# Kernel tuning notes

Measured on AMD Instinct MI355X. Metric: run time of the kernel, lower is better.

The kernel has to match this reference:

```python
import math
import jax, jax.numpy as jnp
import numpy as np

B, S, D = 2, 1024, 4096
H, DH = 32, 128


def setup_inputs() -> dict:
    key = jax.random.key(0)
    ks = jax.random.split(key, 8)
    scale = 1.0 / math.sqrt(D)
    return {
        "hidden_q": jax.random.normal(ks[0], (B, S, D), jnp.float32),
        "hidden_kv": jax.random.normal(ks[1], (B, S, D), jnp.float32),
        "attention_mask": jax.random.randint(ks[2], (B, S, S), 0, 2) > 0,
        "position_bias": jax.random.normal(ks[3], (B, H, S, S), jnp.float32),
        "Wq": jax.random.normal(ks[4], (D, H * DH), jnp.float32) * scale,
        "Wk": jax.random.normal(ks[5], (D, H * DH), jnp.float32) * scale,
        "Wv": jax.random.normal(ks[6], (D, H * DH), jnp.float32) * scale,
        "Wo": jax.random.normal(ks[7], (H * DH, D), jnp.float32) * scale,
    }


def reference(hidden_q, hidden_kv, attention_mask, position_bias, Wq, Wk, Wv, Wo):
    b, len_q, _ = hidden_q.shape
    len_k = hidden_kv.shape[1]
    # projections -> [B, H, S, DH]
    q = (hidden_q @ Wq).reshape(b, len_q, H, DH).transpose(0, 2, 1, 3)
    k = (hidden_kv @ Wk).reshape(b, len_k, H, DH).transpose(0, 2, 1, 3)
    v = (hidden_kv @ Wv).reshape(b, len_k, H, DH).transpose(0, 2, 1, 3)
    # scores [B, H, Q, K]
    score = jnp.einsum("bhqd,bhkd->bhqk", q, k) / math.sqrt(DH)
    score = score + position_bias
    mask = attention_mask[:, None, :, :]  # [B,1,Q,K]
    score = jnp.where(mask, score, -jnp.inf)
    probs = jax.nn.softmax(score, axis=-1)
    probs = jnp.where(mask, probs, 0.0)  # post-softmax mask (also kills NaN rows)
    ctx = jnp.einsum("bhqk,bhkd->bhqd", probs, v)
    ctx = ctx.transpose(0, 2, 1, 3).reshape(b, len_q, H * DH)
    out = ctx @ Wo
    return out
```

## Files before the change

### kernel.cpp

```cpp
#include <hip/hip_runtime.h>
#include <stdint.h>


#define B_  2
#define S_  1024
#define D_  4096
#define H_  32
#define DH_ 128
#define M_  (B_ * S_)
#define KSTR 8192

typedef __attribute__((ext_vector_type(8))) short bf16x8;
typedef __attribute__((ext_vector_type(8))) unsigned short u16x8;
typedef __attribute__((ext_vector_type(4))) float f32x4;

static __device__ __forceinline__ unsigned short f32_to_bf16(float f) {
    unsigned int x = __float_as_uint(f);
    x += 0x7fffu + ((x >> 16) & 1u);
    return (unsigned short)(x >> 16);
}

static __device__ __forceinline__ f32x4 mfma16(bf16x8 a, bf16x8 b, f32x4 c) {
    return __builtin_amdgcn_mfma_f32_16x16x32_bf16(a, b, c, 0, 0, 0);
}

#if defined(__has_builtin)
#if __has_builtin(__builtin_amdgcn_global_load_lds)
#define HAVE_GLOAD_LDS 1
#endif
#endif

#ifdef HAVE_GLOAD_LDS
#define GLD16(g, lbase, lane)                                                  \
    __builtin_amdgcn_global_load_lds(                                          \
        (const __attribute__((address_space(1))) void*)(g),                    \
        (__attribute__((address_space(3))) void*)(lbase), 16, 0, 0)
#else
#define GLD16(g, lbase, lane)                                                  \
    do { *(bf16x8*)((unsigned short*)(lbase) + (size_t)(lane) * 8) =           \
             *(const bf16x8*)(g); } while (0)
#endif

__global__ void detect_mask_kernel(const unsigned char* __restrict__ m, int* flag) {
    int l = threadIdx.x;
    uint4 v = ((const uint4*)m)[l];
    unsigned int ww[4] = {v.x, v.y, v.z, v.w};
    int nz_hi = 0, nz_lo01 = 0;
#pragma unroll
    for (int wi = 0; wi < 4; ++wi)
#pragma unroll
        for (int bi = 0; bi < 4; ++bi) {
            unsigned int byte = (ww[wi] >> (bi * 8)) & 0xffu;
            if (byte && bi != 0) nz_hi = 1;
            if (byte && bi <= 1) nz_lo01 = 1;
        }
    int any_hi = __any(nz_hi);
    int any_lo01 = __any(nz_lo01);
    if (l == 0) *flag = (!any_hi) ? 1 : ((!any_lo01) ? 2 : 0);
}

__global__ void canon_mask_kernel(const void* __restrict__ m, const int* __restrict__ flag,
                                  unsigned char* __restrict__ out, int n) {
    int i = blockIdx.x * 256 + threadIdx.x;
    if (i >= n) return;
    int f = *flag;
    unsigned char v;
    if (f == 1)      v = (unsigned char)(((const int*)m)[i] != 0);
    else if (f == 2) v = (unsigned char)(((const float*)m)[i] != 0.0f);
    else             v = (unsigned char)(((const unsigned char*)m)[i] != 0);
    out[i] = v;
}

__global__ void cvt2_bf16_kernel(const float* __restrict__ a, const float* __restrict__ b,
                                 unsigned short* __restrict__ oa, unsigned short* __restrict__ ob) {
    int i = blockIdx.x * 256 + threadIdx.x;
    const int n4 = (B_ * S_ * D_) / 4;
    const float* src = (i < n4) ? a : b;
    unsigned short* dst = (i < n4) ? oa : ob;
    int j = (i < n4) ? i : i - n4;
    float4 v = ((const float4*)src)[j];
    ushort4 o;
    o.x = f32_to_bf16(v.x); o.y = f32_to_bf16(v.y);
    o.z = f32_to_bf16(v.z); o.w = f32_to_bf16(v.w);
    ((ushort4*)dst)[j] = o;
}

__global__ __launch_bounds__(256) void transpose_all_kernel(
        const float* __restrict__ Wq, const float* __restrict__ Wk,
        const float* __restrict__ Wv, const float* __restrict__ Wo,
        unsigned short* __restrict__ WTq, unsigned short* __restrict__ WTkv,
        unsigned short* __restrict__ WTo) {
    __shared__ unsigned short lds[64][65];
    int which = blockIdx.x >> 12;
    int bid = blockIdx.x & 4095;
    const float* W = (which == 0) ? Wq : (which == 1) ? Wk : (which == 2) ? Wv : Wo;
    unsigned short* WT = (which == 0) ? WTq
                       : (which == 1) ? WTkv
                       : (which == 2) ? (WTkv + (size_t)4096 * 4096)
                                      : WTo;
    int bx = bid & 63;
    int by = bid >> 6;
    int t = threadIdx.x;
    int tr = t >> 4;
    int tc = (t & 15) * 4;
#pragma unroll
    for (int p = 0; p < 4; ++p) {
        int r = p * 16 + tr;
        float4 v = *(const float4*)(W + (size_t)(by * 64 + r) * D_ + bx * 64 + tc);
        lds[r][tc + 0] = f32_to_bf16(v.x);
        lds[r][tc + 1] = f32_to_bf16(v.y);
        lds[r][tc + 2] = f32_to_bf16(v.z);
        lds[r][tc + 3] = f32_to_bf16(v.w);
    }
    __syncthreads();
    int wn = t >> 3;
    int k0 = (t & 7) * 8;
#pragma unroll
    for (int p2 = 0; p2 < 2; ++p2) {
        int n = p2 * 32 + wn;
        u16x8 o;
#pragma unroll
        for (int j = 0; j < 8; ++j) o[j] = lds[k0 + j][n];
        *(u16x8*)(WT + (size_t)(bx * 64 + n) * D_ + by * 64 + k0) = o;
    }
}

__global__ __launch_bounds__(256) void vt_kernel(const unsigned short* __restrict__ KV,
                                                 unsigned short* __restrict__ Vtw) {
    __shared__ unsigned short lds[64][72];
    int bid = blockIdx.x;
    int dt = bid & 1;
    int st = (bid >> 1) & 15;
    int h  = (bid >> 5) & 31;
    int b  = bid >> 10;
    int t = threadIdx.x;
    int r = t >> 2;
    int c0 = (t & 3) * 16;
    const unsigned short* src =
        KV + (size_t)(b * S_ + st * 64 + r) * KSTR + 4096 + h * DH_ + dt * 64 + c0;
    bf16x8 v0 = *(const bf16x8*)(src);
    bf16x8 v1 = *(const bf16x8*)(src + 8);
    *(bf16x8*)&lds[r][c0] = v0;
    *(bf16x8*)&lds[r][c0 + 8] = v1;
    __syncthreads();
    unsigned short tmp[16];
#pragma unroll
    for (int i = 0; i < 16; ++i) tmp[i] = lds[c0 + i][r];
    unsigned short* dst =
        Vtw + ((size_t)((b * H_ + h) * DH_ + dt * 64 + r)) * S_ + st * 64 + c0;
    *(bf16x8*)dst = *(bf16x8*)&tmp[0];
    *(bf16x8*)(dst + 8) = *(bf16x8*)&tmp[8];
}

__device__ __forceinline__ void gemm_core(const unsigned short* __restrict__ A,
                                          const unsigned short* __restrict__ BT,
                                          void* __restrict__ C, int out_f32,
                                          int m0, int n0, int cstride,
                                          int koff, int NT, char* ldsc) {
    const int t = threadIdx.x;
    const int w = t >> 6, l = t & 63;
    const int lr = l & 15, lg = l >> 4;
    const int wmh = w >> 2;
    const int walf = w & 3;
    const int wm = wmh << 7;
    const int wn = walf << 6;

    const int ca0 = lg ^ (lr & 7);
    const int aoff0 = lr * 128 + (ca0 << 4);
    const int aoff1 = lr * 128 + ((ca0 ^ 4) << 4);
    const int boff0 = ((walf & 1) * 64 + lr) * 128 + (ca0 << 4);
    const int boff1 = ((walf & 1) * 64 + lr) * 128 + ((ca0 ^ 4) << 4);

    const int srow = t >> 3;
    const int sch = (t & 7) ^ (srow & 7);
    const size_t soff0 = (size_t)srow * 4096 + (size_t)(sch << 3);
    const size_t soff1 = soff0 + (size_t)64 * 4096;
    const int ldso = w << 10;

    f32x4 ac[8][4];
    f32x4 vzero = {0.f, 0.f, 0.f, 0.f};
#pragma unroll
    for (int i = 0; i < 8; ++i)
#pragma unroll
        for (int j = 0; j < 4; ++j) ac[i][j] = vzero;

#define STAGE_ELEM(E, SS)                                                      \
    do {                                                                       \
        int er_ = (E) & 3;                                                     \
        const unsigned short* mb_ = (er_ < 2)                                  \
            ? A + (size_t)(m0 + ((er_ & 1) << 7)) * 4096                       \
            : BT + (size_t)(n0 + ((er_ & 1) << 7)) * 4096;                     \
        mb_ += (size_t)((((E) >> 2) << 6) + koff);                             \
        char* d0_ = ldsc + (SS) * 16384 + ldso;                                \
        GLD16(mb_ + soff0, d0_, l);                                            \
        GLD16(mb_ + soff1, d0_ + 8192, l);                                     \
    } while (0)

#pragma unroll
    for (int e = 0; e < 6; ++e) STAGE_ELEM(e, e);

    const int NT4 = NT << 2;
    int E = 6, ss = 6, s0 = 0;
    bf16x8 bfr[4][2];

#pragma unroll 1
    for (int tau = 0; tau < NT; ++tau) {
        int sA = s0 + wmh;             if (sA >= 10) sA -= 10;
        int sB = s0 + 2 + (walf >> 1); if (sB >= 10) sB -= 10;
        const char* pA0 = ldsc + sA * 16384 + aoff0;
        const char* pA1 = ldsc + sA * 16384 + aoff1;
        const char* pB0 = ldsc + sB * 16384 + boff0;
        const char* pB1 = ldsc + sB * 16384 + boff1;
#pragma unroll
        for (int r = 0; r < 4; ++r) {
            if (r == 0) {
                if (tau == NT - 1)
                    asm volatile("s_waitcnt vmcnt(0)" ::: "memory");
                else
                    asm volatile("s_waitcnt vmcnt(4)" ::: "memory");
            }
            __builtin_amdgcn_s_barrier();
            asm volatile("" ::: "memory");
            if (r == 0) {
#pragma unroll
                for (int nf = 0; nf < 4; ++nf) {
                    bfr[nf][0] = *(const bf16x8*)(pB0 + nf * 2048);
                    bfr[nf][1] = *(const bf16x8*)(pB1 + nf * 2048);
                }
            }
            bf16x8 af[2][2];
            int mfb = r << 1;
#pragma unroll
            for (int j = 0; j < 2; ++j) {
                af[j][0] = *(const bf16x8*)(pA0 + (mfb + j) * 2048);
                af[j][1] = *(const bf16x8*)(pA1 + (mfb + j) * 2048);
            }
            if (E < NT4) STAGE_ELEM(E, ss);
            ++E; ss = (ss == 9) ? 0 : ss + 1;
            __builtin_amdgcn_s_setprio(1);
#pragma unroll
            for (int j = 0; j < 2; ++j)
#pragma unroll
                for (int nf = 0; nf < 4; ++nf) {
                    ac[mfb + j][nf] = mfma16(af[j][0], bfr[nf][0], ac[mfb + j][nf]);
                    ac[mfb + j][nf] = mfma16(af[j][1], bfr[nf][1], ac[mfb + j][nf]);
                }
            __builtin_amdgcn_s_setprio(0);
        }
        s0 += 4; if (s0 >= 10) s0 -= 10;
    }
#undef STAGE_ELEM

#pragma unroll
    for (int mf = 0; mf < 8; ++mf)
#pragma unroll
        for (int nf = 0; nf < 4; ++nf)
#pragma unroll
            for (int q = 0; q < 4; ++q) {
                int row = m0 + wm + mf * 16 + lg * 4 + q;
                int col = n0 + wn + nf * 16 + lr;
                if (out_f32)
                    ((float*)C)[(size_t)row * cstride + col] = ac[mf][nf][q];
                else
                    ((unsigned short*)C)[(size_t)row * cstride + col] = f32_to_bf16(ac[mf][nf][q]);
            }
}

__global__ __launch_bounds__(512, 1) void gemm_qkv_kernel(
        const unsigned short* __restrict__ Aq, const unsigned short* __restrict__ Bq,
        float* __restrict__ Pq,
        const unsigned short* __restrict__ Akv, const unsigned short* __restrict__ Bkv,
        unsigned short* __restrict__ Ckv) {
    __shared__ char ldsbuf[10 * 16384];
    int bid = blockIdx.x;
    if (bid < 256) {
        int bm = bid & 7, bn = bid >> 3;
        gemm_core(Akv, Bkv, Ckv, 0, bm << 8, bn << 8, 8192, 0, 64, ldsbuf);
    } else {
        int e = bid - 256;
        int bm = e & 7;
        int rest = e >> 3;
        int bn = rest & 15;
        int ks = rest >> 4;
        gemm_core(Aq, Bq, Pq + (size_t)ks * M_ * D_, 1, bm << 8, bn << 8, 4096,
                  ks * 2048, 32, ldsbuf);
    }
}

__global__ void reduce_q_kernel(const float* __restrict__ P, unsigned short* __restrict__ out) {
    int i = blockIdx.x * 256 + threadIdx.x;
    float4 a = ((const float4*)P)[i];
    float4 b = ((const float4*)(P + (size_t)M_ * D_))[i];
    ushort4 o;
    o.x = f32_to_bf16(a.x + b.x); o.y = f32_to_bf16(a.y + b.y);
    o.z = f32_to_bf16(a.z + b.z); o.w = f32_to_bf16(a.w + b.w);
    ((ushort4*)out)[i] = o;
}

__global__ __launch_bounds__(512, 1) void gemm_o_kernel(
        const unsigned short* __restrict__ A, const unsigned short* __restrict__ BT,
        float* __restrict__ P) {
    __shared__ char ldsbuf[10 * 16384];
    int bid = blockIdx.x;
    int bm = bid & 7;
    int rest = bid >> 3;
    int bn = rest & 15;
    int ks = rest >> 4;
    gemm_core(A, BT, P + (size_t)ks * M_ * D_, 1, bm << 8, bn << 8, 4096,
              ks * 2048, 32, ldsbuf);
}

__global__ void reduce_o_kernel(const float* __restrict__ P, float* __restrict__ out) {
    int i = blockIdx.x * 256 + threadIdx.x;
    float4 a = ((const float4*)P)[i];
    float4 b = ((const float4*)(P + (size_t)M_ * D_))[i];
    float4 o; o.x = a.x + b.x; o.y = a.y + b.y; o.z = a.z + b.z; o.w = a.w + b.w;
    ((float4*)out)[i] = o;
}

#define NEGF (-1e30f)
__global__ __launch_bounds__(256, 2) void attn_kernel(const unsigned short* __restrict__ Qw,
                                                      const unsigned short* __restrict__ KV,
                                                      const unsigned short* __restrict__ Vtw,
                                                      const float* __restrict__ bias,
                                                      const unsigned char* __restrict__ maskc,
                                                      unsigned short* __restrict__ ctx) {
    __shared__ unsigned short Kbuf[2][64 * 128];
    __shared__ unsigned short Vbuf[2][128 * 64];
    __shared__ unsigned short Plds[4][16 * 72];

    int x = blockIdx.x;
    int xcd = x & 7;
    int rest = x >> 3;
    int qt = rest & 15;
    int gq = rest >> 4;
    int g = gq * 8 + xcd;
    int b = g >> 5, h = g & 31;

    int t = threadIdx.x, w = t >> 6, l = t & 63;
    int lr = l & 15, lg = l >> 4;
    int q0 = (qt << 6) + (w << 4);

    bf16x8 qf[4];
    const unsigned short* Qp = Qw + ((size_t)(b * S_ + q0 + lr)) * D_ + h * DH_ + lg * 8;
#pragma unroll
    for (int kf = 0; kf < 4; ++kf) qf[kf] = *(const bf16x8*)(Qp + kf * 32);

    f32x4 o[8];
    f32x4 vzero = {0.f, 0.f, 0.f, 0.f};
#pragma unroll
    for (int i = 0; i < 8; ++i) o[i] = vzero;
    float m_run = NEGF, l_run = 0.f;

    const float* biasp = bias + (((size_t)(b * H_ + h)) << 20)
                              + (((size_t)(q0 + lr)) << 10);
    const unsigned char* mp = maskc + ((size_t)b << 20)
                              + (((size_t)(q0 + lr)) << 10);
    const unsigned short* Kg = KV + (size_t)(b * S_) * KSTR + h * DH_;
    const unsigned short* Vg = Vtw + (((size_t)(b * H_ + h)) * DH_) * S_;

    float4 br0[4], br1[4];
    unsigned int mr0[4], mr1[4];

#define STAGE_KV(KT, BUF)                                                          \
    do { int kv0_ = (KT) << 6;                                                     \
        _Pragma("unroll")                                                          \
        for (int c = 0; c < 4; ++c) {                                              \
            int seg = (w << 2) + c;                                                \
            int krow = (seg << 2) + (l >> 4);                                      \
            int kch = (l & 15) ^ (krow & 7);                                       \
            GLD16(Kg + (size_t)(kv0_ + krow) * KSTR + (kch << 3),                  \
                  &Kbuf[BUF][seg << 9], l);                                        \
            int vrow = (seg << 3) + (l >> 3);                                      \
            int vch = (l & 7) ^ (vrow & 7);                                        \
            GLD16(Vg + (size_t)vrow * S_ + kv0_ + (vch << 3),                      \
                  &Vbuf[BUF][seg << 9], l);                                        \
        }                                                                          \
    } while (0)

#define LOAD_BM(BR, MR, KT)                                                        \
    do { int kv0_ = (KT) << 6;                                                     \
        _Pragma("unroll")                                                          \
        for (int nb = 0; nb < 4; ++nb) {                                           \
            BR[nb] = *(const float4*)(biasp + kv0_ + (nb << 4) + (lg << 2));       \
            MR[nb] = *(const unsigned int*)(mp + kv0_ + (nb << 4) + (lg << 2));    \
        }                                                                          \
    } while (0)

#define COMPUTE(BUF, BR, MR)                                                       \
    do {                                                                           \
        f32x4 s_[4];                                                               \
        __builtin_amdgcn_s_setprio(1);                                             \
        _Pragma("unroll")                                                          \
        for (int nb = 0; nb < 4; ++nb) {                                           \
            s_[nb] = vzero;                                                        \
            int krow = (nb << 4) + lr;                                             \
            _Pragma("unroll")                                                      \
            for (int kf = 0; kf < 4; ++kf) {                                       \
                int ba = ((krow << 8) + (((kf << 5) + (lg << 3)) << 1))            \
                         ^ ((krow & 7) << 4);                                      \
                bf16x8 kfr = *(const bf16x8*)((const char*)Kbuf[BUF] + ba);        \
                s_[nb] = mfma16(kfr, qf[kf], s_[nb]);                              \
            }                                                                      \
        }                                                                          \
        __builtin_amdgcn_s_setprio(0);                                             \
        float sv[4][4];                                                            \
        _Pragma("unroll")                                                          \
        for (int nb = 0; nb < 4; ++nb) {                                           \
            float bb[4] = {BR[nb].x, BR[nb].y, BR[nb].z, BR[nb].w};                \
            _Pragma("unroll")                                                      \
            for (int r = 0; r < 4; ++r) {                                          \
                float x2 = fmaf(s_[nb][r], 0.08838834764831845f, bb[r]);           \
                sv[nb][r] = ((MR[nb] >> (r * 8)) & 0xffu) ? x2 : NEGF;             \
            }                                                                      \
        }                                                                          \
        float mt = sv[0][0];                                                       \
        _Pragma("unroll")                                                          \
        for (int nb = 0; nb < 4; ++nb)                                             \
            _Pragma("unroll")                                                      \
            for (int r = 0; r < 4; ++r) mt = fmaxf(mt, sv[nb][r]);                 \
        mt = fmaxf(mt, __shfl_xor(mt, 16, 64));                                    \
        mt = fmaxf(mt, __shfl_xor(mt, 32, 64));                                    \
        float mn = fmaxf(m_run, mt);                                               \
        float al = __expf(m_run - mn);                                             \
        m_run = mn;                                                                \
        float rs = 0.f;                                                            \
        _Pragma("unroll")                                                          \
        for (int nb = 0; nb < 4; ++nb)                                             \
            _Pragma("unroll")                                                      \
            for (int r = 0; r < 4; ++r) {                                          \
                sv[nb][r] = __expf(sv[nb][r] - m_run);                             \
                rs += sv[nb][r];                                                   \
            }                                                                      \
        rs += __shfl_xor(rs, 16, 64);                                              \
        rs += __shfl_xor(rs, 32, 64);                                              \
        l_run = l_run * al + rs;                                                   \
        float alm[4];                                                              \
        _Pragma("unroll")                                                          \
        for (int r = 0; r < 4; ++r) alm[r] = __shfl(al, (lg << 2) + r, 64);        \
        _Pragma("unroll")                                                          \
        for (int nb2 = 0; nb2 < 8; ++nb2) {                                        \
            o[nb2][0] *= alm[0]; o[nb2][1] *= alm[1];                              \
            o[nb2][2] *= alm[2]; o[nb2][3] *= alm[3];                              \
        }                                                                          \
        _Pragma("unroll")                                                          \
        for (int nb = 0; nb < 4; ++nb)                                             \
            _Pragma("unroll")                                                      \
            for (int r = 0; r < 4; ++r)                                            \
                Plds[w][lr * 72 + (nb << 4) + (lg << 2) + r] = f32_to_bf16(sv[nb][r]); \
        __builtin_amdgcn_s_setprio(1);                                             \
        _Pragma("unroll")                                                          \
        for (int kf2 = 0; kf2 < 2; ++kf2) {                                        \
            bf16x8 pf = *(const bf16x8*)&Plds[w][lr * 72 + (kf2 << 5) + (lg << 3)]; \
            _Pragma("unroll")                                                      \
            for (int nb2 = 0; nb2 < 8; ++nb2) {                                    \
                int dh = (nb2 << 4) + lr;                                          \
                int ba = ((dh << 7) + (((kf2 << 5) + (lg << 3)) << 1))             \
                         ^ ((dh & 7) << 4);                                        \
                bf16x8 vf = *(const bf16x8*)((const char*)Vbuf[BUF] + ba);         \
                o[nb2] = mfma16(pf, vf, o[nb2]);                                   \
            }                                                                      \
        }                                                                          \
        __builtin_amdgcn_s_setprio(0);                                             \
    } while (0)

    STAGE_KV(0, 0);
    LOAD_BM(br0, mr0, 0);

#pragma unroll 1
    for (int kt = 0; kt < 16; kt += 2) {
        __syncthreads();
        STAGE_KV(kt + 1, 1);
        LOAD_BM(br1, mr1, kt + 1);
        COMPUTE(0, br0, mr0);
        __syncthreads();
        if (kt < 14) {
            STAGE_KV(kt + 2, 0);
            LOAD_BM(br0, mr0, kt + 2);
        }
        COMPUTE(1, br1, mr1);
    }

    float lm[4];
#pragma unroll
    for (int r = 0; r < 4; ++r) lm[r] = __shfl(l_run, (lg << 2) + r, 64);
#pragma unroll
    for (int r = 0; r < 4; ++r) {
        float inv = lm[r] > 0.f ? 1.0f / lm[r] : 0.f;
        int q = q0 + (lg << 2) + r;
        unsigned short* cp = ctx + ((size_t)(b * S_ + q)) * D_ + h * DH_ + lr;
#pragma unroll
        for (int nb2 = 0; nb2 < 8; ++nb2)
            cp[nb2 * 16] = f32_to_bf16(o[nb2][r] * inv);
    }
#undef STAGE_KV
#undef LOAD_BM
#undef COMPUTE
}

extern "C" void kernel_launch(void* const* d_in, const int* in_sizes, int n_in,
                              void* d_out, int out_size, void* d_ws, size_t ws_size,
                              hipStream_t stream) {
    const float* hq   = (const float*)d_in[0];
    const float* hkv  = (const float*)d_in[1];
    const void*  mask = d_in[2];
    const float* bias = (const float*)d_in[3];
    const float* Wq   = (const float*)d_in[4];
    const float* Wk   = (const float*)d_in[5];
    const float* Wv   = (const float*)d_in[6];
    const float* Wo   = (const float*)d_in[7];
    float* out = (float*)d_out;

    char* ws = (char*)d_ws;
    unsigned char* mask_c = (unsigned char*)ws;
    int* flag             = (int*)(ws + (2u << 20));
    unsigned short* hq_b  = (unsigned short*)(ws + (2u << 20) + 4096);
    unsigned short* hkv_b = hq_b + ((size_t)1 << 23);
    unsigned short* WTq   = hkv_b + ((size_t)1 << 23);
    unsigned short* WTo   = WTq + ((size_t)1 << 24);
    unsigned short* WTkv  = WTo + ((size_t)1 << 24);
    unsigned short* Qws   = WTkv + ((size_t)1 << 25);
    unsigned short* KVws  = Qws + ((size_t)1 << 23);
    unsigned short* Cws   = KVws + ((size_t)1 << 24);
    unsigned short* Vtw   = Cws + ((size_t)1 << 23);
    float* Pws            = (float*)(Vtw + ((size_t)1 << 23));

    detect_mask_kernel<<<1, 64, 0, stream>>>((const unsigned char*)mask, flag);
    canon_mask_kernel<<<8192, 256, 0, stream>>>(mask, flag, mask_c, B_ * S_ * S_);
    cvt2_bf16_kernel<<<16384, 256, 0, stream>>>(hq, hkv, hq_b, hkv_b);
    transpose_all_kernel<<<16384, 256, 0, stream>>>(Wq, Wk, Wv, Wo, WTq, WTkv, WTo);

    gemm_qkv_kernel<<<512, 512, 0, stream>>>(hq_b, WTq, Pws, hkv_b, WTkv, KVws);
    reduce_q_kernel<<<(M_ * D_) / 1024, 256, 0, stream>>>(Pws, Qws);

    vt_kernel<<<B_ * H_ * 16 * 2, 256, 0, stream>>>(KVws, Vtw);
    attn_kernel<<<B_ * H_ * (S_ / 64), 256, 0, stream>>>(Qws, KVws, Vtw, bias, mask_c, Cws);

    gemm_o_kernel<<<256, 512, 0, stream>>>(Cws, WTo, Pws);
    reduce_o_kernel<<<(M_ * D_) / 1024, 256, 0, stream>>>(Pws, out);
}
```

Baseline: 500.0 us.

## Process two query tiles per attention block and merge small prep kernels

New measurement: 590.8 us. 1.18x slower.

```diff
diff --git a/kernel.cpp b/kernel.cpp
--- a/kernel.cpp
+++ b/kernel.cpp
@@ -41,29 +41,30 @@
              *(const bf16x8*)(g); } while (0)
 #endif
 
-__global__ void detect_mask_kernel(const unsigned char* __restrict__ m, int* flag) {
-    int l = threadIdx.x;
-    uint4 v = ((const uint4*)m)[l];
-    unsigned int ww[4] = {v.x, v.y, v.z, v.w};
-    int nz_hi = 0, nz_lo01 = 0;
-#pragma unroll
-    for (int wi = 0; wi < 4; ++wi)
-#pragma unroll
-        for (int bi = 0; bi < 4; ++bi) {
-            unsigned int byte = (ww[wi] >> (bi * 8)) & 0xffu;
-            if (byte && bi != 0) nz_hi = 1;
-            if (byte && bi <= 1) nz_lo01 = 1;
-        }
-    int any_hi = __any(nz_hi);
-    int any_lo01 = __any(nz_lo01);
-    if (l == 0) *flag = (!any_hi) ? 1 : ((!any_lo01) ? 2 : 0);
-}
-
-__global__ void canon_mask_kernel(const void* __restrict__ m, const int* __restrict__ flag,
+__global__ void canon_mask_kernel(const void* __restrict__ m,
                                   unsigned char* __restrict__ out, int n) {
-    int i = blockIdx.x * 256 + threadIdx.x;
+    __shared__ int sflag;
+    int t = threadIdx.x;
+    if (t < 64) {
+        uint4 v = ((const uint4*)m)[t];
+        unsigned int ww[4] = {v.x, v.y, v.z, v.w};
+        int nz_hi = 0, nz_lo01 = 0;
+#pragma unroll
+        for (int wi = 0; wi < 4; ++wi)
+#pragma unroll
+            for (int bi = 0; bi < 4; ++bi) {
+                unsigned int byte = (ww[wi] >> (bi * 8)) & 0xffu;
+                if (byte && bi != 0) nz_hi = 1;
+                if (byte && bi <= 1) nz_lo01 = 1;
+            }
+        int any_hi = __any(nz_hi);
+        int any_lo01 = __any(nz_lo01);
+        if (t == 0) sflag = (!any_hi) ? 1 : ((!any_lo01) ? 2 : 0);
+    }
+    __syncthreads();
+    int f = sflag;
+    int i = blockIdx.x * 256 + t;
     if (i >= n) return;
-    int f = *flag;
     unsigned char v;
     if (f == 1)      v = (unsigned char)(((const int*)m)[i] != 0);
     else if (f == 2) v = (unsigned char)(((const float*)m)[i] != 0.0f);
@@ -125,31 +126,43 @@
     }
 }
 
-__global__ __launch_bounds__(256) void vt_kernel(const unsigned short* __restrict__ KV,
-                                                 unsigned short* __restrict__ Vtw) {
+__global__ __launch_bounds__(256) void vtrq_kernel(const unsigned short* __restrict__ KV,
+                                                   unsigned short* __restrict__ Vtw,
+                                                   const float* __restrict__ P,
+                                                   unsigned short* __restrict__ Qout) {
     __shared__ unsigned short lds[64][72];
     int bid = blockIdx.x;
-    int dt = bid & 1;
-    int st = (bid >> 1) & 15;
-    int h  = (bid >> 5) & 31;
-    int b  = bid >> 10;
     int t = threadIdx.x;
-    int r = t >> 2;
-    int c0 = (t & 3) * 16;
-    const unsigned short* src =
-        KV + (size_t)(b * S_ + st * 64 + r) * KSTR + 4096 + h * DH_ + dt * 64 + c0;
-    bf16x8 v0 = *(const bf16x8*)(src);
-    bf16x8 v1 = *(const bf16x8*)(src + 8);
-    *(bf16x8*)&lds[r][c0] = v0;
-    *(bf16x8*)&lds[r][c0 + 8] = v1;
-    __syncthreads();
-    unsigned short tmp[16];
-#pragma unroll
-    for (int i = 0; i < 16; ++i) tmp[i] = lds[c0 + i][r];
-    unsigned short* dst =
-        Vtw + ((size_t)((b * H_ + h) * DH_ + dt * 64 + r)) * S_ + st * 64 + c0;
-    *(bf16x8*)dst = *(bf16x8*)&tmp[0];
-    *(bf16x8*)(dst + 8) = *(bf16x8*)&tmp[8];
+    if (bid < 2048) {
+        int dt = bid & 1;
+        int st = (bid >> 1) & 15;
+        int h  = (bid >> 5) & 31;
+        int b  = bid >> 10;
+        int r = t >> 2;
+        int c0 = (t & 3) * 16;
+        const unsigned short* src =
+            KV + (size_t)(b * S_ + st * 64 + r) * KSTR + 4096 + h * DH_ + dt * 64 + c0;
+        bf16x8 v0 = *(const bf16x8*)(src);
+        bf16x8 v1 = *(const bf16x8*)(src + 8);
+        *(bf16x8*)&lds[r][c0] = v0;
+        *(bf16x8*)&lds[r][c0 + 8] = v1;
+        __syncthreads();
+        unsigned short tmp[16];
+#pragma unroll
+        for (int i = 0; i < 16; ++i) tmp[i] = lds[c0 + i][r];
+        unsigned short* dst =
+            Vtw + ((size_t)((b * H_ + h) * DH_ + dt * 64 + r)) * S_ + st * 64 + c0;
+        *(bf16x8*)dst = *(bf16x8*)&tmp[0];
+        *(bf16x8*)(dst + 8) = *(bf16x8*)&tmp[8];
+    } else {
+        int i = (bid - 2048) * 256 + t;
+        float4 a = ((const float4*)P)[i];
+        float4 b = ((const float4*)(P + (size_t)M_ * D_))[i];
+        ushort4 o;
+        o.x = f32_to_bf16(a.x + b.x); o.y = f32_to_bf16(a.y + b.y);
+        o.z = f32_to_bf16(a.z + b.z); o.w = f32_to_bf16(a.w + b.w);
+        ((ushort4*)Qout)[i] = o;
+    }
 }
 
 __device__ __forceinline__ void gemm_core(const unsigned short* __restrict__ A,
@@ -287,16 +300,6 @@
     }
 }
 
-__global__ void reduce_q_kernel(const float* __restrict__ P, unsigned short* __restrict__ out) {
-    int i = blockIdx.x * 256 + threadIdx.x;
-    float4 a = ((const float4*)P)[i];
-    float4 b = ((const float4*)(P + (size_t)M_ * D_))[i];
-    ushort4 o;
-    o.x = f32_to_bf16(a.x + b.x); o.y = f32_to_bf16(a.y + b.y);
-    o.z = f32_to_bf16(a.z + b.z); o.w = f32_to_bf16(a.w + b.w);
-    ((ushort4*)out)[i] = o;
-}
-
 __global__ __launch_bounds__(512, 1) void gemm_o_kernel(
         const unsigned short* __restrict__ A, const unsigned short* __restrict__ BT,
         float* __restrict__ P) {
@@ -332,8 +335,8 @@
     int x = blockIdx.x;
     int xcd = x & 7;
     int rest = x >> 3;
-    int qt = rest & 15;
-    int gq = rest >> 4;
+    int qt = rest & 7;
+    int gq = rest >> 3;
     int g = gq * 8 + xcd;
     int b = g >> 5, h = g & 31;
 
@@ -341,26 +344,31 @@
     int lr = l & 15, lg = l >> 4;
     int q0 = (qt << 6) + (w << 4);
 
-    bf16x8 qf[4];
+    bf16x8 qfA[4], qfB[4];
     const unsigned short* Qp = Qw + ((size_t)(b * S_ + q0 + lr)) * D_ + h * DH_ + lg * 8;
 #pragma unroll
-    for (int kf = 0; kf < 4; ++kf) qf[kf] = *(const bf16x8*)(Qp + kf * 32);
-
-    f32x4 o[8];
+    for (int kf = 0; kf < 4; ++kf) {
+        qfA[kf] = *(const bf16x8*)(Qp + kf * 32);
+        qfB[kf] = *(const bf16x8*)(Qp + (size_t)512 * D_ + kf * 32);
+    }
+
+    f32x4 oA[8], oB[8];
     f32x4 vzero = {0.f, 0.f, 0.f, 0.f};
 #pragma unroll
-    for (int i = 0; i < 8; ++i) o[i] = vzero;
-    float m_run = NEGF, l_run = 0.f;
-
-    const float* biasp = bias + (((size_t)(b * H_ + h)) << 20)
-                              + (((size_t)(q0 + lr)) << 10);
-    const unsigned char* mp = maskc + ((size_t)b << 20)
-                              + (((size_t)(q0 + lr)) << 10);
+    for (int i = 0; i < 8; ++i) { oA[i] = vzero; oB[i] = vzero; }
+    float mA = NEGF, lA = 0.f, mB = NEGF, lB = 0.f;
+
+    const float* biaspA = bias + (((size_t)(b * H_ + h)) << 20)
+                               + (((size_t)(q0 + lr)) << 10);
+    const float* biaspB = biaspA + ((size_t)512 << 10);
+    const unsigned char* mpA = maskc + ((size_t)b << 20)
+                               + (((size_t)(q0 + lr)) << 10);
+    const unsigned char* mpB = mpA + ((size_t)512 << 10);
     const unsigned short* Kg = KV + (size_t)(b * S_) * KSTR + h * DH_;
     const unsigned short* Vg = Vtw + (((size_t)(b * H_ + h)) * DH_) * S_;
 
-    float4 br0[4], br1[4];
-    unsigned int mr0[4], mr1[4];
+    float4 brA0[4], brA1[4], brB0[4], brB1[4];
+    unsigned int mrA0[4], mrA1[4], mrB0[4], mrB1[4];
 
 #define STAGE_KV(KT, BUF)                                                          \
     do { int kv0_ = (KT) << 6;                                                     \
@@ -378,16 +386,16 @@
         }                                                                          \
     } while (0)
 
-#define LOAD_BM(BR, MR, KT)                                                        \
+#define LOAD_BM(BR, MR, BP, MP, KT)                                                \
     do { int kv0_ = (KT) << 6;                                                     \
         _Pragma("unroll")                                                          \
         for (int nb = 0; nb < 4; ++nb) {                                           \
-            BR[nb] = *(const float4*)(biasp + kv0_ + (nb << 4) + (lg << 2));       \
-            MR[nb] = *(const unsigned int*)(mp + kv0_ + (nb << 4) + (lg << 2));    \
+            BR[nb] = *(const float4*)(BP + kv0_ + (nb << 4) + (lg << 2));          \
+            MR[nb] = *(const unsigned int*)(MP + kv0_ + (nb << 4) + (lg << 2));    \
         }                                                                          \
     } while (0)
 
-#define COMPUTE(BUF, BR, MR)                                                       \
+#define COMPUTE(BUF, BR, MR, QF, O, MRUN, LRUN)                                    \
     do {                                                                           \
         f32x4 s_[4];                                                               \
         __builtin_amdgcn_s_setprio(1);                                             \
@@ -400,7 +408,7 @@
                 int ba = ((krow << 8) + (((kf << 5) + (lg << 3)) << 1))            \
                          ^ ((krow & 7) << 4);                                      \
                 bf16x8 kfr = *(const bf16x8*)((const char*)Kbuf[BUF] + ba);        \
-                s_[nb] = mfma16(kfr, qf[kf], s_[nb]);                              \
+                s_[nb] = mfma16(kfr, QF[kf], s_[nb]);                              \
             }                                                                      \
         }                                                                          \
         __builtin_amdgcn_s_setprio(0);                                             \
@@ -421,27 +429,27 @@
             for (int r = 0; r < 4; ++r) mt = fmaxf(mt, sv[nb][r]);                 \
         mt = fmaxf(mt, __shfl_xor(mt, 16, 64));                                    \
         mt = fmaxf(mt, __shfl_xor(mt, 32, 64));                                    \
-        float mn = fmaxf(m_run, mt);                                               \
-        float al = __expf(m_run - mn);                                             \
-        m_run = mn;                                                                \
+        float mn = fmaxf(MRUN, mt);                                                \
+        float al = __expf(MRUN - mn);                                              \
+        MRUN = mn;                                                                 \
         float rs = 0.f;                                                            \
         _Pragma("unroll")                                                          \
         for (int nb = 0; nb < 4; ++nb)                                             \
             _Pragma("unroll")                                                      \
             for (int r = 0; r < 4; ++r) {                                          \
-                sv[nb][r] = __expf(sv[nb][r] - m_run);                             \
+                sv[nb][r] = __expf(sv[nb][r] - MRUN);                              \
                 rs += sv[nb][r];                                                   \
             }                                                                      \
         rs += __shfl_xor(rs, 16, 64);                                              \
         rs += __shfl_xor(rs, 32, 64);                                              \
-        l_run = l_run * al + rs;                                                   \
+        LRUN = LRUN * al + rs;                                                     \
         float alm[4];                                                              \
         _Pragma("unroll")                                                          \
         for (int r = 0; r < 4; ++r) alm[r] = __shfl(al, (lg << 2) + r, 64);        \
         _Pragma("unroll")                                                          \
         for (int nb2 = 0; nb2 < 8; ++nb2) {                                        \
-            o[nb2][0] *= alm[0]; o[nb2][1] *= alm[1];                              \
-            o[nb2][2] *= alm[2]; o[nb2][3] *= alm[3];                              \
+            O[nb2][0] *= alm[0]; O[nb2][1] *= alm[1];                              \
+            O[nb2][2] *= alm[2]; O[nb2][3] *= alm[3];                              \
         }                                                                          \
         _Pragma("unroll")                                                          \
         for (int nb = 0; nb < 4; ++nb)                                             \
@@ -458,40 +466,52 @@
                 int ba = ((dh << 7) + (((kf2 << 5) + (lg << 3)) << 1))             \
                          ^ ((dh & 7) << 4);                                        \
                 bf16x8 vf = *(const bf16x8*)((const char*)Vbuf[BUF] + ba);         \
-                o[nb2] = mfma16(pf, vf, o[nb2]);                                   \
+                O[nb2] = mfma16(pf, vf, O[nb2]);                                   \
             }                                                                      \
         }                                                                          \
         __builtin_amdgcn_s_setprio(0);                                             \
     } while (0)
 
     STAGE_KV(0, 0);
-    LOAD_BM(br0, mr0, 0);
+    LOAD_BM(brA0, mrA0, biaspA, mpA, 0);
+    LOAD_BM(brB0, mrB0, biaspB, mpB, 0);
 
 #pragma unroll 1
     for (int kt = 0; kt < 16; kt += 2) {
         __syncthreads();
         STAGE_KV(kt + 1, 1);
-        LOAD_BM(br1, mr1, kt + 1);
-        COMPUTE(0, br0, mr0);
+        LOAD_BM(brA1, mrA1, biaspA, mpA, kt + 1);
+        LOAD_BM(brB1, mrB1, biaspB, mpB, kt + 1);
+        COMPUTE(0, brA0, mrA0, qfA, oA, mA, lA);
+        COMPUTE(0, brB0, mrB0, qfB, oB, mB, lB);
         __syncthreads();
         if (kt < 14) {
             STAGE_KV(kt + 2, 0);
-            LOAD_BM(br0, mr0, kt + 2);
+            LOAD_BM(brA0, mrA0, biaspA, mpA, kt + 2);
+            LOAD_BM(brB0, mrB0, biaspB, mpB, kt + 2);
         }
-        COMPUTE(1, br1, mr1);
-    }
-
-    float lm[4];
-#pragma unroll
-    for (int r = 0; r < 4; ++r) lm[r] = __shfl(l_run, (lg << 2) + r, 64);
+        COMPUTE(1, brA1, mrA1, qfA, oA, mA, lA);
+        COMPUTE(1, brB1, mrB1, qfB, oB, mB, lB);
+    }
+
+    float lmA[4], lmB[4];
 #pragma unroll
     for (int r = 0; r < 4; ++r) {
-        float inv = lm[r] > 0.f ? 1.0f / lm[r] : 0.f;
+        lmA[r] = __shfl(lA, (lg << 2) + r, 64);
+        lmB[r] = __shfl(lB, (lg << 2) + r, 64);
+    }
+#pragma unroll
+    for (int r = 0; r < 4; ++r) {
+        float invA = lmA[r] > 0.f ? 1.0f / lmA[r] : 0.f;
+        float invB = lmB[r] > 0.f ? 1.0f / lmB[r] : 0.f;
         int q = q0 + (lg << 2) + r;
-        unsigned short* cp = ctx + ((size_t)(b * S_ + q)) * D_ + h * DH_ + lr;
-#pragma unroll
-        for (int nb2 = 0; nb2 < 8; ++nb2)
-            cp[nb2 * 16] = f32_to_bf16(o[nb2][r] * inv);
+        unsigned short* cpA = ctx + ((size_t)(b * S_ + q)) * D_ + h * DH_ + lr;
+        unsigned short* cpB = cpA + (size_t)512 * D_;
+#pragma unroll
+        for (int nb2 = 0; nb2 < 8; ++nb2) {
+            cpA[nb2 * 16] = f32_to_bf16(oA[nb2][r] * invA);
+            cpB[nb2 * 16] = f32_to_bf16(oB[nb2][r] * invB);
+        }
     }
 #undef STAGE_KV
 #undef LOAD_BM
@@ -513,7 +533,6 @@
 
     char* ws = (char*)d_ws;
     unsigned char* mask_c = (unsigned char*)ws;
-    int* flag             = (int*)(ws + (2u << 20));
     unsigned short* hq_b  = (unsigned short*)(ws + (2u << 20) + 4096);
     unsigned short* hkv_b = hq_b + ((size_t)1 << 23);
     unsigned short* WTq   = hkv_b + ((size_t)1 << 23);
@@ -525,16 +544,14 @@
     unsigned short* Vtw   = Cws + ((size_t)1 << 23);
     float* Pws            = (float*)(Vtw + ((size_t)1 << 23));
 
-    detect_mask_kernel<<<1, 64, 0, stream>>>((const unsigned char*)mask, flag);
-    canon_mask_kernel<<<8192, 256, 0, stream>>>(mask, flag, mask_c, B_ * S_ * S_);
+    canon_mask_kernel<<<8192, 256, 0, stream>>>(mask, mask_c, B_ * S_ * S_);
     cvt2_bf16_kernel<<<16384, 256, 0, stream>>>(hq, hkv, hq_b, hkv_b);
     transpose_all_kernel<<<16384, 256, 0, stream>>>(Wq, Wk, Wv, Wo, WTq, WTkv, WTo);
 
     gemm_qkv_kernel<<<512, 512, 0, stream>>>(hq_b, WTq, Pws, hkv_b, WTkv, KVws);
-    reduce_q_kernel<<<(M_ * D_) / 1024, 256, 0, stream>>>(Pws, Qws);
-
-    vt_kernel<<<B_ * H_ * 16 * 2, 256, 0, stream>>>(KVws, Vtw);
-    attn_kernel<<<B_ * H_ * (S_ / 64), 256, 0, stream>>>(Qws, KVws, Vtw, bias, mask_c, Cws);
+    vtrq_kernel<<<10240, 256, 0, stream>>>(KVws, Vtw, Pws, Qws);
+
+    attn_kernel<<<512, 256, 0, stream>>>(Qws, KVws, Vtw, bias, mask_c, Cws);
 
     gemm_o_kernel<<<256, 512, 0, stream>>>(Cws, WTo, Pws);
     reduce_o_kernel<<<(M_ * D_) / 1024, 256, 0, stream>>>(Pws, out);
```
